# Kernel optimization log

Hardware: AMD Instinct MI355X
Metric: run time of the kernel (lower is better)

The kernel has to match this reference:

```python
import jax, jax.numpy as jnp
import numpy as np

KH = KW = 3
PAD = 1


def _conv2d(x, w, b):
    y = jax.lax.conv_general_dilated(
        x, w, window_strides=(1, 1), padding=((PAD, PAD), (PAD, PAD)),
        dimension_numbers=("NCHW", "OIHW", "NCHW"))
    return y + b[None, :, None, None]


def _bilinear_sample_one(img, ys, xs):
    # img: [C,H,W]; ys,xs: [K,h,w] absolute sampling coords; zeros outside.
    C, H, W = img.shape
    flat = img.reshape(C, H * W)
    y0 = jnp.floor(ys)
    x0 = jnp.floor(xs)
    wy = ys - y0
    wx = xs - x0

    def gather(yi, xi):
        valid = (yi >= 0) & (yi <= H - 1) & (xi >= 0) & (xi <= W - 1)
        yc = jnp.clip(yi, 0, H - 1).astype(jnp.int32)
        xc = jnp.clip(xi, 0, W - 1).astype(jnp.int32)
        idx = (yc * W + xc).reshape(-1)
        v = jnp.take(flat, idx, axis=1).reshape((C,) + yi.shape)
        return v * valid.astype(img.dtype)

    v00 = gather(y0, x0)
    v01 = gather(y0, x0 + 1)
    v10 = gather(y0 + 1, x0)
    v11 = gather(y0 + 1, x0 + 1)
    return (v00 * (1 - wy) * (1 - wx) + v01 * (1 - wy) * wx
            + v10 * wy * (1 - wx) + v11 * wy * wx)  # [C,K,h,w]


def deform_conv2d(x, offset, weight, bias):
    # x: [B,C,H,W]; offset: [B,2K,h,w] with (dy,dx) per tap; stride 1, pad 1.
    B, C, H, W = x.shape
    h, w = offset.shape[2], offset.shape[3]
    K = KH * KW
    off = offset.reshape(B, K, 2, h, w)
    ky = (jnp.arange(K) // KW - PAD).astype(x.dtype)  # tap row displacement
    kx = (jnp.arange(K) % KW - PAD).astype(x.dtype)
    ii = jnp.arange(h, dtype=x.dtype)[None, :, None]
    jj = jnp.arange(w, dtype=x.dtype)[None, None, :]
    ys = ii - PAD + ky[:, None, None] + off[:, :, 0]  # [B,K,h,w]
    xs = jj - PAD + kx[:, None, None] + off[:, :, 1]
    sampled = jax.vmap(_bilinear_sample_one)(x, ys, xs)  # [B,C,K,h,w]
    Co = weight.shape[0]
    out = jnp.einsum('ock,bckhw->bohw', weight.reshape(Co, C, K), sampled)
    return out + bias[None, :, None, None]


def setup_inputs() -> dict:
    key = jax.random.key(0)
    ks = jax.random.split(key, 5)
    B, C, H, W = 4, 64, 128, 128
    x = jax.random.normal(ks[0], (B, C, H, W), dtype=jnp.float32)
    w_off = jax.random.normal(ks[1], (4, C, KH, KW), dtype=jnp.float32) * 0.05
    b_off = jnp.zeros((4,), dtype=jnp.float32)
    weight = jax.random.normal(ks[2], (C, C, KH, KW), dtype=jnp.float32) * 0.05
    bias = jnp.zeros((C,), dtype=jnp.float32)
    # base_offset: canonical 3x3 tap displacements, layout (dy,dx) per tap.
    ky = np.repeat(np.arange(KH) - PAD, KW).astype(np.float32)
    kx = np.tile(np.arange(KW) - PAD, KH).astype(np.float32)
    base = np.stack([ky, kx], axis=1).reshape(-1)  # [18]
    base_offset = jnp.asarray(np.broadcast_to(base[None, :, None, None], (1, 18, H, W)).copy())
    idx = np.arange(18)
    mask1 = jnp.asarray(idx % 2 == 0)  # y coords -> scale1
    mask2 = jnp.asarray(idx % 2 == 1)  # x coords -> scale2
    return {"x": x, "w_off": w_off, "b_off": b_off, "weight": weight,
            "bias": bias, "base_offset": base_offset, "mask1": mask1, "mask2": mask2}


def reference(x, w_off, b_off, weight, bias, base_offset, mask1, mask2):
    off = _conv2d(x, w_off, b_off)  # [B,4,h,w]
    scale1 = jax.nn.relu(off[:, 2:3]) + 1.0  # [B,1,h,w]
    scale2 = jax.nn.relu(off[:, 3:4]) + 1.0
    shift = jnp.tile(off[:, :2], (1, KH * KW, 1, 1))  # [B,18,h,w]
    # scaled_offset[:, mask1] = base*scale1 ; scaled_offset[:, mask2] = base*scale2
    scale_full = jnp.where(mask1[None, :, None, None], scale1, scale2)  # [B,18,h,w]
    offset = base_offset * scale_full - base_offset + shift
    return deform_conv2d(x, offset, weight, bias)
```

## Files before the change

### kernel.cpp

```cpp
#include <hip/hip_runtime.h>

#define Hd 128
#define Wd 128
#define Cd 64
#define COd 64
#define Bd 4
#define HWd (Hd*Wd)

typedef __attribute__((ext_vector_type(8))) _Float16 half8;
typedef __attribute__((ext_vector_type(2))) _Float16 h2;
typedef __attribute__((ext_vector_type(4))) float    f32x4;

__device__ __align__(16) _Float16 g_wh[COd*576];
__device__ __align__(16) _Float16 g_woffh[16*576];
__device__ __align__(16) unsigned short g_xt[(size_t)Bd*HWd*Cd];

static __device__ __forceinline__ unsigned cvtpkh(float lo, float hi) {
    unsigned r;
    asm("v_cvt_pkrtz_f16_f32 %0, %1, %2" : "=v"(r) : "v"(lo), "v"(hi));
    return r;
}
static __device__ __forceinline__ h2 ash2(unsigned u) {
    union { unsigned u; h2 h; } x; x.u = u; return x.h;
}
static __device__ __forceinline__ unsigned ash2u(h2 h) {
    union { h2 h; unsigned u; } x; x.h = h; return x.u;
}

__global__ __launch_bounds__(256) void k_prep(const float* __restrict__ x,
                                              const float* __restrict__ weight,
                                              const float* __restrict__ w_off) {
    int bid = blockIdx.x;
    if (bid < 512) {
        int b = bid >> 7, y = bid & 127;
        int px = threadIdx.x & 127;
        int h  = threadIdx.x >> 7;
        const float* xb = x + (size_t)b*Cd*HWd + y*Wd + px;
        unsigned short* ob = g_xt + ((size_t)(b*HWd) + y*Wd + px)*Cd + h*32;
        #pragma unroll
        for (int oct = 0; oct < 4; ++oct) {
            unsigned pk[4];
            #pragma unroll
            for (int e = 0; e < 4; ++e) {
                float v0 = xb[(size_t)(h*32 + oct*8 + 2*e    )*HWd];
                float v1 = xb[(size_t)(h*32 + oct*8 + 2*e + 1)*HWd];
                pk[e] = cvtpkh(v0, v1);
            }
            *(uint4*)(ob + oct*8) = make_uint4(pk[0], pk[1], pk[2], pk[3]);
        }
    } else if (bid < 656) {
        int g = (bid - 512)*256 + threadIdx.x;
        if (g < COd*576) {
            int co = g / 576, k = g % 576;
            int t = k >> 6, c = k & 63;
            g_wh[g] = (_Float16)weight[(co*Cd + c)*9 + t];
        }
    } else {
        int g = (bid - 656)*256 + threadIdx.x;
        if (g < 16*576) {
            int row = g / 576, k = g % 576;
            int t = k >> 6, c = k & 63;
            g_woffh[g] = (row < 4) ? (_Float16)w_off[(row*Cd + c)*9 + t] : (_Float16)0.f;
        }
    }
}

#define GATHER(T, U00, U01, U10, U11, H00, H01, H10, H11)                         \
    {                                                                             \
        float ys = (float)(i - 1) + (float)((T)/3 - 1)*s1v + off0;                \
        float xs = (float)(jA - 1) + (float)((T)%3 - 1)*s2v + off1;               \
        float y0f = floorf(ys), x0f = floorf(xs);                                 \
        float wy = ys - y0f, wx = xs - x0f;                                       \
        float vy0 = (y0f >=  0.f && y0f <= 127.f) ? 1.f : 0.f;                    \
        float vy1 = (y0f >= -1.f && y0f <= 126.f) ? 1.f : 0.f;                    \
        float vx0 = (x0f >=  0.f && x0f <= 127.f) ? 1.f : 0.f;                    \
        float vx1 = (x0f >= -1.f && x0f <= 126.f) ? 1.f : 0.f;                    \
        float w00 = (1.f-wy)*(1.f-wx)*vy0*vx0, w01 = (1.f-wy)*wx*vy0*vx1;         \
        float w10 = wy*(1.f-wx)*vy1*vx0,       w11 = wy*wx*vy1*vx1;               \
        H00 = ash2(cvtpkh(w00, w00)); H01 = ash2(cvtpkh(w01, w01));               \
        H10 = ash2(cvtpkh(w10, w10)); H11 = ash2(cvtpkh(w11, w11));               \
        int iy0 = min(max((int)y0f,     0), 127), iy1 = min(max((int)y0f+1,0),127);\
        int ix0 = min(max((int)x0f,     0), 127), ix1 = min(max((int)x0f+1,0),127);\
        U00 = *(const uint4*)(xb + (size_t)(iy0*Wd + ix0)*Cd + oct*8);            \
        U01 = *(const uint4*)(xb + (size_t)(iy0*Wd + ix1)*Cd + oct*8);            \
        U10 = *(const uint4*)(xb + (size_t)(iy1*Wd + ix0)*Cd + oct*8);            \
        U11 = *(const uint4*)(xb + (size_t)(iy1*Wd + ix1)*Cd + oct*8);            \
    }

#define PACK_STORE(BUF, U00, U01, U10, U11, H00, H01, H10, H11)                   \
    {                                                                             \
        unsigned a00[4] = {U00.x,U00.y,U00.z,U00.w};                              \
        unsigned a01[4] = {U01.x,U01.y,U01.z,U01.w};                              \
        unsigned a10[4] = {U10.x,U10.y,U10.z,U10.w};                              \
        unsigned a11[4] = {U11.x,U11.y,U11.z,U11.w};                              \
        unsigned pk[4];                                                           \
        _Pragma("unroll")                                                         \
        for (int e = 0; e < 4; ++e) {                                             \
            h2 r = ash2(a00[e])*H00 + ash2(a01[e])*H01                            \
                 + ash2(a10[e])*H10 + ash2(a11[e])*H11;                           \
            pk[e] = ash2u(r);                                                     \
        }                                                                         \
        lds_b[(((BUF)*2 + par)*2 + nt)*64 + slotA] = make_uint4(pk[0],pk[1],pk[2],pk[3]); \
    }

__global__ __launch_bounds__(256) void k_deform(const float* __restrict__ b_off,
                                                const float* __restrict__ bias,
                                                float* __restrict__ out) {
    __shared__ uint4  lds_b[2*2*2*64];
    __shared__ float4 lds_off[32];
    int orig = blockIdx.x;
    int xcd = orig & 7, slotB = orig >> 3;
    int g = xcd*2 + (slotB >> 7);
    int s = slotB & 127;
    int b = g >> 2;
    int i = (g & 3)*32 + (s >> 2);
    int j0 = (s & 3) << 5;

    int w = threadIdx.x >> 6, l = threadIdx.x & 63;
    const unsigned short* xb = g_xt + (size_t)b*HWd*Cd;

    if (w < 2) {
        int pc = l & 15, q = l >> 4;
        int j  = j0 + w*16 + pc;
        const _Float16* arow = g_woffh + pc*576 + q*8;
        f32x4 acc = {0.f, 0.f, 0.f, 0.f};
        #pragma unroll
        for (int t = 0; t < 9; ++t) {
            int yy = i + t/3 - 1, xx = j + t%3 - 1;
            bool ok = (yy >= 0) & (yy <= 127) & (xx >= 0) & (xx <= 127);
            const unsigned short* p = xb + (size_t)(yy*Wd + xx)*Cd + q*8;
            uint4 u0 = ok ? *(const uint4*)p        : make_uint4(0,0,0,0);
            uint4 u1 = ok ? *(const uint4*)(p + 32) : make_uint4(0,0,0,0);
            half8 a0 = *(const half8*)(arow + (2*t    )*32);
            half8 a1 = *(const half8*)(arow + (2*t + 1)*32);
            acc = __builtin_amdgcn_mfma_f32_16x16x32_f16(a0, *(half8*)&u0, acc, 0, 0, 0);
            acc = __builtin_amdgcn_mfma_f32_16x16x32_f16(a1, *(half8*)&u1, acc, 0, 0, 0);
        }
        if (q == 0) {
            float o0 = acc[0] + b_off[0];
            float o1 = acc[1] + b_off[1];
            float o2 = fmaxf(acc[2] + b_off[2], 0.f) + 1.f;
            float o3 = fmaxf(acc[3] + b_off[3], 0.f) + 1.f;
            lds_off[w*16 + pc] = make_float4(o0, o1, o2, o3);
        }
    }
    __syncthreads();

    int oct = l & 7, px8 = l >> 3;
    int pxl = w*8 + px8;
    int jA  = j0 + pxl;
    int nt = pxl >> 4, pcA = pxl & 15, qA = oct & 3, par = oct >> 2;
    int slotA = (pcA ^ (qA << 1)) + (qA << 4);
    int pcB = l & 15, qB = l >> 4;
    int physl = (pcB ^ (qB << 1)) + (qB << 4);
    const _Float16* wrow = g_wh + (size_t)(w*16 + pcB)*576 + qB*8;

    float4 o4 = lds_off[pxl];
    float off0 = o4.x, off1 = o4.y, s1v = o4.z, s2v = o4.w;

    f32x4 acc0 = {0.f,0.f,0.f,0.f};
    f32x4 acc1 = {0.f,0.f,0.f,0.f};

    uint4 gc00, gc01, gc10, gc11, gn00, gn01, gn10, gn11;
    h2 hc00, hc01, hc10, hc11, hn00, hn01, hn10, hn11;

    GATHER(0, gc00, gc01, gc10, gc11, hc00, hc01, hc10, hc11);

    #pragma unroll
    for (int t = 0; t < 9; ++t) {
        if (t < 8) {
            GATHER(t+1, gn00, gn01, gn10, gn11, hn00, hn01, hn10, hn11);
        }
        PACK_STORE(t & 1, gc00, gc01, gc10, gc11, hc00, hc01, hc10, hc11);
        __syncthreads();
        {
            half8 a0 = *(const half8*)(wrow + (2*t    )*32);
            half8 a1 = *(const half8*)(wrow + (2*t + 1)*32);
            half8 b00 = *(const half8*)&lds_b[(((t&1)*2 + 0)*2 + 0)*64 + physl];
            half8 b01 = *(const half8*)&lds_b[(((t&1)*2 + 0)*2 + 1)*64 + physl];
            half8 b10 = *(const half8*)&lds_b[(((t&1)*2 + 1)*2 + 0)*64 + physl];
            half8 b11 = *(const half8*)&lds_b[(((t&1)*2 + 1)*2 + 1)*64 + physl];
            acc0 = __builtin_amdgcn_mfma_f32_16x16x32_f16(a0, b00, acc0, 0, 0, 0);
            acc1 = __builtin_amdgcn_mfma_f32_16x16x32_f16(a0, b01, acc1, 0, 0, 0);
            acc0 = __builtin_amdgcn_mfma_f32_16x16x32_f16(a1, b10, acc0, 0, 0, 0);
            acc1 = __builtin_amdgcn_mfma_f32_16x16x32_f16(a1, b11, acc1, 0, 0, 0);
        }
        if (t < 8) {
            gc00 = gn00; gc01 = gn01; gc10 = gn10; gc11 = gn11;
            hc00 = hn00; hc01 = hn01; hc10 = hn10; hc11 = hn11;
        }
    }

    #pragma unroll
    for (int rr = 0; rr < 4; ++rr) {
        int co = w*16 + qB*4 + rr;
        float bco = bias[co];
        size_t base = ((size_t)(b*COd + co)*Hd + i)*Wd + j0;
        out[base + pcB]      = acc0[rr] + bco;
        out[base + 16 + pcB] = acc1[rr] + bco;
    }
}

extern "C" void kernel_launch(void* const* d_in, const int* in_sizes, int n_in,
                              void* d_out, int out_size, void* d_ws, size_t ws_size,
                              hipStream_t stream) {
    const float* x      = (const float*)d_in[0];
    const float* w_off  = (const float*)d_in[1];
    const float* b_off  = (const float*)d_in[2];
    const float* weight = (const float*)d_in[3];
    const float* bias   = (const float*)d_in[4];
    float* out = (float*)d_out;

    hipLaunchKernelGGL(k_prep,   dim3(692),  dim3(256), 0, stream, x, weight, w_off);
    hipLaunchKernelGGL(k_deform, dim3(2048), dim3(256), 0, stream, b_off, bias, out);
}
```

Measured before the change: 62.18 us.

## Split offset convolution into separate kernel with LDS-staged row reuse

Moves the offset-predicting 3x3 conv out of the deform kernel into a new kernel, k_offs. Each block stages three input rows in LDS, computes offsets and scales for a full 128-pixel row with all four waves, and writes them to a global float4 buffer. The deform kernel now reads its per-pixel offsets from that buffer. This drops a block-wide sync and the two-wave prologue, during which half the waves sat idle, and cuts redundant global reads of neighbour rows. The cost is an extra kernel launch and a small global round-trip for the offsets.

```diff
diff --git a/kernel.cpp b/kernel.cpp
--- a/kernel.cpp
+++ b/kernel.cpp
@@ -13,6 +13,7 @@
 
 __device__ __align__(16) _Float16 g_wh[COd*576];
 __device__ __align__(16) _Float16 g_woffh[16*576];
+__device__ float4 g_offs[Bd*HWd];
 __device__ __align__(16) unsigned short g_xt[(size_t)Bd*HWd*Cd];
 
 static __device__ __forceinline__ unsigned cvtpkh(float lo, float hi) {
@@ -65,6 +66,65 @@
     }
 }
 
+__global__ __launch_bounds__(256) void k_offs(const float* __restrict__ b_off) {
+    __shared__ uint4 lds_x[3*8*128];
+    int orig = blockIdx.x;
+    int xcd = orig & 7, slot = orig >> 3;
+    int g = xcd*2 + (slot >> 5);
+    int b = g >> 2;
+    int i = (g & 3)*32 + (slot & 31);
+
+    int tid = threadIdx.x;
+    const unsigned short* xb = g_xt + (size_t)b*HWd*Cd;
+
+    #pragma unroll
+    for (int rr = 0; rr < 3; ++rr) {
+        int y = i + rr - 1;
+        bool rv = (y >= 0) && (y <= 127);
+        #pragma unroll
+        for (int k = 0; k < 4; ++k) {
+            int n = k*256 + tid;
+            int px = n >> 3, c = n & 7;
+            uint4 v = rv ? *(const uint4*)(xb + (size_t)(y*Wd + px)*Cd + c*8)
+                         : make_uint4(0, 0, 0, 0);
+            lds_x[(rr*8 + c)*128 + px] = v;
+        }
+    }
+    __syncthreads();
+
+    int w = tid >> 6, l = tid & 63;
+    int pc = l & 15, q = l >> 4;
+    const _Float16* arow = g_woffh + pc*576 + q*8;
+    float bo0 = b_off[0], bo1 = b_off[1], bo2 = b_off[2], bo3 = b_off[3];
+
+    #pragma unroll
+    for (int tile = 0; tile < 2; ++tile) {
+        int j = (w*2 + tile)*16 + pc;
+        f32x4 acc = {0.f, 0.f, 0.f, 0.f};
+        #pragma unroll
+        for (int t = 0; t < 9; ++t) {
+            int dy = t/3, dx = t%3 - 1;
+            int px = j + dx;
+            bool ok = (px >= 0) && (px <= 127);
+            int pxc = min(max(px, 0), 127);
+            uint4 u0 = lds_x[(dy*8 + q    )*128 + pxc];
+            uint4 u1 = lds_x[(dy*8 + q + 4)*128 + pxc];
+            if (!ok) { u0 = make_uint4(0,0,0,0); u1 = make_uint4(0,0,0,0); }
+            half8 a0 = *(const half8*)(arow + (2*t    )*32);
+            half8 a1 = *(const half8*)(arow + (2*t + 1)*32);
+            acc = __builtin_amdgcn_mfma_f32_16x16x32_f16(a0, *(half8*)&u0, acc, 0, 0, 0);
+            acc = __builtin_amdgcn_mfma_f32_16x16x32_f16(a1, *(half8*)&u1, acc, 0, 0, 0);
+        }
+        if (q == 0) {
+            float o0 = acc[0] + bo0;
+            float o1 = acc[1] + bo1;
+            float o2 = fmaxf(acc[2] + bo2, 0.f) + 1.f;
+            float o3 = fmaxf(acc[3] + bo3, 0.f) + 1.f;
+            g_offs[(b*Hd + i)*Wd + j] = make_float4(o0, o1, o2, o3);
+        }
+    }
+}
+
 #define GATHER(T, U00, U01, U10, U11, H00, H01, H10, H11)                         \
     {                                                                             \
         float ys = (float)(i - 1) + (float)((T)/3 - 1)*s1v + off0;                \
@@ -103,11 +163,9 @@
         lds_b[(((BUF)*2 + par)*2 + nt)*64 + slotA] = make_uint4(pk[0],pk[1],pk[2],pk[3]); \
     }
 
-__global__ __launch_bounds__(256) void k_deform(const float* __restrict__ b_off,
-                                                const float* __restrict__ bias,
+__global__ __launch_bounds__(256) void k_deform(const float* __restrict__ bias,
                                                 float* __restrict__ out) {
-    __shared__ uint4  lds_b[2*2*2*64];
-    __shared__ float4 lds_off[32];
+    __shared__ uint4 lds_b[2*2*2*64];
     int orig = blockIdx.x;
     int xcd = orig & 7, slotB = orig >> 3;
     int g = xcd*2 + (slotB >> 7);
@@ -117,35 +175,6 @@
     int j0 = (s & 3) << 5;
 
     int w = threadIdx.x >> 6, l = threadIdx.x & 63;
-    const unsigned short* xb = g_xt + (size_t)b*HWd*Cd;
-
-    if (w < 2) {
-        int pc = l & 15, q = l >> 4;
-        int j  = j0 + w*16 + pc;
-        const _Float16* arow = g_woffh + pc*576 + q*8;
-        f32x4 acc = {0.f, 0.f, 0.f, 0.f};
-        #pragma unroll
-        for (int t = 0; t < 9; ++t) {
-            int yy = i + t/3 - 1, xx = j + t%3 - 1;
-            bool ok = (yy >= 0) & (yy <= 127) & (xx >= 0) & (xx <= 127);
-            const unsigned short* p = xb + (size_t)(yy*Wd + xx)*Cd + q*8;
-            uint4 u0 = ok ? *(const uint4*)p        : make_uint4(0,0,0,0);
-            uint4 u1 = ok ? *(const uint4*)(p + 32) : make_uint4(0,0,0,0);
-            half8 a0 = *(const half8*)(arow + (2*t    )*32);
-            half8 a1 = *(const half8*)(arow + (2*t + 1)*32);
-            acc = __builtin_amdgcn_mfma_f32_16x16x32_f16(a0, *(half8*)&u0, acc, 0, 0, 0);
-            acc = __builtin_amdgcn_mfma_f32_16x16x32_f16(a1, *(half8*)&u1, acc, 0, 0, 0);
-        }
-        if (q == 0) {
-            float o0 = acc[0] + b_off[0];
-            float o1 = acc[1] + b_off[1];
-            float o2 = fmaxf(acc[2] + b_off[2], 0.f) + 1.f;
-            float o3 = fmaxf(acc[3] + b_off[3], 0.f) + 1.f;
-            lds_off[w*16 + pc] = make_float4(o0, o1, o2, o3);
-        }
-    }
-    __syncthreads();
-
     int oct = l & 7, px8 = l >> 3;
     int pxl = w*8 + px8;
     int jA  = j0 + pxl;
@@ -155,7 +184,8 @@
     int physl = (pcB ^ (qB << 1)) + (qB << 4);
     const _Float16* wrow = g_wh + (size_t)(w*16 + pcB)*576 + qB*8;
 
-    float4 o4 = lds_off[pxl];
+    const unsigned short* xb = g_xt + (size_t)b*HWd*Cd;
+    float4 o4 = g_offs[(b*Hd + i)*Wd + jA];
     float off0 = o4.x, off1 = o4.y, s1v = o4.z, s2v = o4.w;
 
     f32x4 acc0 = {0.f,0.f,0.f,0.f};
@@ -212,5 +242,6 @@
     float* out = (float*)d_out;
 
     hipLaunchKernelGGL(k_prep,   dim3(692),  dim3(256), 0, stream, x, weight, w_off);
-    hipLaunchKernelGGL(k_deform, dim3(2048), dim3(256), 0, stream, b_off, bias, out);
-}
+    hipLaunchKernelGGL(k_offs,   dim3(512),  dim3(256), 0, stream, b_off);
+    hipLaunchKernelGGL(k_deform, dim3(2048), dim3(256), 0, stream, bias, out);
+}
```

New measurement: 51.83 us (median of 2 runs). -16.6%, faster.

## Fuse offset conv with x transpose into separate kernel, drop it from deform

Applied to the files above, without the earlier changes.

Moves the offset-predicting 3x3 conv out of the deform kernel into a new kernel that also does the NCHW-to-NHWC fp16 transpose of x. That kernel stages a 3-row halo tile of x in LDS, writes the centre row to the transposed buffer, and runs the offset MFMA from LDS rather than global memory. Offsets go through a global float4 buffer, so the deform kernel loses its prologue conv and one barrier. The cost is an extra launch, and each x row is loaded three times (halo) from the fp32 NCHW input.

```diff
diff --git a/kernel.cpp b/kernel.cpp
--- a/kernel.cpp
+++ b/kernel.cpp
@@ -13,6 +13,7 @@
 
 __device__ __align__(16) _Float16 g_wh[COd*576];
 __device__ __align__(16) _Float16 g_woffh[16*576];
+__device__ float4 g_offs[Bd*HWd];
 __device__ __align__(16) unsigned short g_xt[(size_t)Bd*HWd*Cd];
 
 static __device__ __forceinline__ unsigned cvtpkh(float lo, float hi) {
@@ -27,41 +28,93 @@
     union { h2 h; unsigned u; } x; x.h = h; return x.u;
 }
 
-__global__ __launch_bounds__(256) void k_prep(const float* __restrict__ x,
-                                              const float* __restrict__ weight,
+__global__ __launch_bounds__(256) void k_prep(const float* __restrict__ weight,
                                               const float* __restrict__ w_off) {
     int bid = blockIdx.x;
-    if (bid < 512) {
-        int b = bid >> 7, y = bid & 127;
-        int px = threadIdx.x & 127;
-        int h  = threadIdx.x >> 7;
-        const float* xb = x + (size_t)b*Cd*HWd + y*Wd + px;
-        unsigned short* ob = g_xt + ((size_t)(b*HWd) + y*Wd + px)*Cd + h*32;
-        #pragma unroll
-        for (int oct = 0; oct < 4; ++oct) {
-            unsigned pk[4];
-            #pragma unroll
-            for (int e = 0; e < 4; ++e) {
-                float v0 = xb[(size_t)(h*32 + oct*8 + 2*e    )*HWd];
-                float v1 = xb[(size_t)(h*32 + oct*8 + 2*e + 1)*HWd];
-                pk[e] = cvtpkh(v0, v1);
-            }
-            *(uint4*)(ob + oct*8) = make_uint4(pk[0], pk[1], pk[2], pk[3]);
-        }
-    } else if (bid < 656) {
-        int g = (bid - 512)*256 + threadIdx.x;
+    if (bid < 144) {
+        int g = bid*256 + threadIdx.x;
         if (g < COd*576) {
             int co = g / 576, k = g % 576;
             int t = k >> 6, c = k & 63;
             g_wh[g] = (_Float16)weight[(co*Cd + c)*9 + t];
         }
     } else {
-        int g = (bid - 656)*256 + threadIdx.x;
+        int g = (bid - 144)*256 + threadIdx.x;
         if (g < 16*576) {
             int row = g / 576, k = g % 576;
             int t = k >> 6, c = k & 63;
             g_woffh[g] = (row < 4) ? (_Float16)w_off[(row*Cd + c)*9 + t] : (_Float16)0.f;
         }
+    }
+}
+
+__global__ __launch_bounds__(256) void k_offs(const float* __restrict__ x,
+                                              const float* __restrict__ b_off) {
+    __shared__ uint4 lds_x[3*8*66];
+    int orig = blockIdx.x;
+    int xcd = orig & 7, slot = orig >> 3;
+    int g = xcd*2 + (slot >> 6);
+    int s = slot & 63;
+    int b  = g >> 2;
+    int i  = (g & 3)*32 + (s >> 1);
+    int j0 = (s & 1) << 6;
+    int tid = threadIdx.x;
+    const float* xb = x + (size_t)b*Cd*HWd;
+
+    for (int base = 0; base < 1584; base += 256) {
+        int n = base + tid;
+        if (n < 1584) {
+            int px = n % 66;
+            int rc = n / 66;
+            int rr = rc >> 3, c = rc & 7;
+            int y  = i + rr - 1;
+            int jj = j0 - 1 + px;
+            unsigned pk[4];
+            if (y >= 0 && y <= 127 && jj >= 0 && jj <= 127) {
+                const float* p = xb + (size_t)(c*8)*HWd + y*Wd + jj;
+                #pragma unroll
+                for (int e = 0; e < 4; ++e) {
+                    float v0 = p[(size_t)(2*e    )*HWd];
+                    float v1 = p[(size_t)(2*e + 1)*HWd];
+                    pk[e] = cvtpkh(v0, v1);
+                }
+            } else { pk[0] = pk[1] = pk[2] = pk[3] = 0u; }
+            lds_x[n] = make_uint4(pk[0], pk[1], pk[2], pk[3]);
+        }
+    }
+    __syncthreads();
+
+    {
+        int n = tid;
+        #pragma unroll
+        for (int k = 0; k < 2; ++k, n += 256) {
+            int px = n >> 3, c = n & 7;
+            uint4 v = lds_x[(8 + c)*66 + (px + 1)];
+            *(uint4*)(g_xt + ((size_t)(b*HWd) + i*Wd + j0 + px)*Cd + c*8) = v;
+        }
+    }
+
+    int w = tid >> 6, l = tid & 63;
+    int pc = l & 15, q = l >> 4;
+    int jl = w*16 + pc;
+    const _Float16* arow = g_woffh + pc*576 + q*8;
+    f32x4 acc = {0.f, 0.f, 0.f, 0.f};
+    #pragma unroll
+    for (int t = 0; t < 9; ++t) {
+        int dy = t/3, dxp = t%3;
+        uint4 u0 = lds_x[(dy*8 + q    )*66 + jl + dxp];
+        uint4 u1 = lds_x[(dy*8 + q + 4)*66 + jl + dxp];
+        half8 a0 = *(const half8*)(arow + (2*t    )*32);
+        half8 a1 = *(const half8*)(arow + (2*t + 1)*32);
+        acc = __builtin_amdgcn_mfma_f32_16x16x32_f16(a0, *(half8*)&u0, acc, 0, 0, 0);
+        acc = __builtin_amdgcn_mfma_f32_16x16x32_f16(a1, *(half8*)&u1, acc, 0, 0, 0);
+    }
+    if (q == 0) {
+        float o0 = acc[0] + b_off[0];
+        float o1 = acc[1] + b_off[1];
+        float o2 = fmaxf(acc[2] + b_off[2], 0.f) + 1.f;
+        float o3 = fmaxf(acc[3] + b_off[3], 0.f) + 1.f;
+        g_offs[(b*Hd + i)*Wd + j0 + jl] = make_float4(o0, o1, o2, o3);
     }
 }
 
@@ -103,11 +156,9 @@
         lds_b[(((BUF)*2 + par)*2 + nt)*64 + slotA] = make_uint4(pk[0],pk[1],pk[2],pk[3]); \
     }
 
-__global__ __launch_bounds__(256) void k_deform(const float* __restrict__ b_off,
-                                                const float* __restrict__ bias,
+__global__ __launch_bounds__(256) void k_deform(const float* __restrict__ bias,
                                                 float* __restrict__ out) {
-    __shared__ uint4  lds_b[2*2*2*64];
-    __shared__ float4 lds_off[32];
+    __shared__ uint4 lds_b[2*2*2*64];
     int orig = blockIdx.x;
     int xcd = orig & 7, slotB = orig >> 3;
     int g = xcd*2 + (slotB >> 7);
@@ -117,35 +168,6 @@
     int j0 = (s & 3) << 5;
 
     int w = threadIdx.x >> 6, l = threadIdx.x & 63;
-    const unsigned short* xb = g_xt + (size_t)b*HWd*Cd;
-
-    if (w < 2) {
-        int pc = l & 15, q = l >> 4;
-        int j  = j0 + w*16 + pc;
-        const _Float16* arow = g_woffh + pc*576 + q*8;
-        f32x4 acc = {0.f, 0.f, 0.f, 0.f};
-        #pragma unroll
-        for (int t = 0; t < 9; ++t) {
-            int yy = i + t/3 - 1, xx = j + t%3 - 1;
-            bool ok = (yy >= 0) & (yy <= 127) & (xx >= 0) & (xx <= 127);
-            const unsigned short* p = xb + (size_t)(yy*Wd + xx)*Cd + q*8;
-            uint4 u0 = ok ? *(const uint4*)p        : make_uint4(0,0,0,0);
-            uint4 u1 = ok ? *(const uint4*)(p + 32) : make_uint4(0,0,0,0);
-            half8 a0 = *(const half8*)(arow + (2*t    )*32);
-            half8 a1 = *(const half8*)(arow + (2*t + 1)*32);
-            acc = __builtin_amdgcn_mfma_f32_16x16x32_f16(a0, *(half8*)&u0, acc, 0, 0, 0);
-            acc = __builtin_amdgcn_mfma_f32_16x16x32_f16(a1, *(half8*)&u1, acc, 0, 0, 0);
-        }
-        if (q == 0) {
-            float o0 = acc[0] + b_off[0];
-            float o1 = acc[1] + b_off[1];
-            float o2 = fmaxf(acc[2] + b_off[2], 0.f) + 1.f;
-            float o3 = fmaxf(acc[3] + b_off[3], 0.f) + 1.f;
-            lds_off[w*16 + pc] = make_float4(o0, o1, o2, o3);
-        }
-    }
-    __syncthreads();
-
     int oct = l & 7, px8 = l >> 3;
     int pxl = w*8 + px8;
     int jA  = j0 + pxl;
@@ -155,7 +177,8 @@
     int physl = (pcB ^ (qB << 1)) + (qB << 4);
     const _Float16* wrow = g_wh + (size_t)(w*16 + pcB)*576 + qB*8;
 
-    float4 o4 = lds_off[pxl];
+    const unsigned short* xb = g_xt + (size_t)b*HWd*Cd;
+    float4 o4 = g_offs[(b*Hd + i)*Wd + jA];
     float off0 = o4.x, off1 = o4.y, s1v = o4.z, s2v = o4.w;
 
     f32x4 acc0 = {0.f,0.f,0.f,0.f};
@@ -211,6 +234,7 @@
     const float* bias   = (const float*)d_in[4];
     float* out = (float*)d_out;
 
-    hipLaunchKernelGGL(k_prep,   dim3(692),  dim3(256), 0, stream, x, weight, w_off);
-    hipLaunchKernelGGL(k_deform, dim3(2048), dim3(256), 0, stream, b_off, bias, out);
-}
+    hipLaunchKernelGGL(k_prep,   dim3(180),  dim3(256), 0, stream, weight, w_off);
+    hipLaunchKernelGGL(k_offs,   dim3(1024), dim3(256), 0, stream, x, b_off);
+    hipLaunchKernelGGL(k_deform, dim3(2048), dim3(256), 0, stream, bias, out);
+}
```

Result: faster. 53.14 us (-14.5%).
